# Kernel optimization log

Measured on AMD Instinct MI355X. Metric: run time of the kernel, lower is better.

The kernel has to match this reference:

```python
import jax, jax.numpy as jnp
import numpy as np

EPS = 1e-5

def layernorm2d(x, w, b):
    # nn.LayerNorm([T, C]): normalize jointly over last two dims, affine shape [T, C]
    mu = jnp.mean(x, axis=(-2, -1), keepdims=True)
    var = jnp.mean(jnp.square(x - mu), axis=(-2, -1), keepdims=True)
    return (x - mu) * jax.lax.rsqrt(var + EPS) * w + b


def setup_inputs() -> dict:
    key = jax.random.key(0)
    ks = jax.random.split(key, 10)
    B, T, C = 64, 512, 512
    s = 0.02
    inputs = jax.random.normal(ks[0], (B, T, C), dtype=jnp.float32)
    ln1_w = jnp.ones((T, C), dtype=jnp.float32)
    ln1_b = jnp.zeros((T, C), dtype=jnp.float32)
    ln2_w = jnp.ones((T, C), dtype=jnp.float32)
    ln2_b = jnp.zeros((T, C), dtype=jnp.float32)
    # TriU: row i holds the Linear(i+1,1) weights for prefix 0..i -> lower-triangular [T,T]
    tri_M = jax.random.normal(ks[1], (T, T), dtype=jnp.float32) * s
    tri_b = jax.random.normal(ks[2], (T,), dtype=jnp.float32) * s
    d1_w = jax.random.normal(ks[3], (C, C), dtype=jnp.float32) * s  # dense_1: out = x @ d1_w.T + d1_b
    d1_b = jax.random.normal(ks[4], (C,), dtype=jnp.float32) * s
    d2_w = jax.random.normal(ks[5], (C, C), dtype=jnp.float32) * s
    d2_b = jax.random.normal(ks[6], (C,), dtype=jnp.float32) * s
    return {"inputs": inputs, "ln1_w": ln1_w, "ln1_b": ln1_b,
            "ln2_w": ln2_w, "ln2_b": ln2_b,
            "tri_M": tri_M, "tri_b": tri_b,
            "d1_w": d1_w, "d1_b": d1_b, "d2_w": d2_w, "d2_b": d2_b}


def reference(inputs, ln1_w, ln1_b, ln2_w, ln2_b, tri_M, tri_b, d1_w, d1_b, d2_w, d2_b):
    # x: [B, T, C]
    x = layernorm2d(inputs, ln1_w, ln1_b)
    # TriU time mixer: out[b,i,c] = sum_{j<=i} M[i,j] * x[b,j,c] + tri_b[i]
    M = jnp.tril(tri_M)
    x = jnp.einsum('it,btc->bic', M, x) + tri_b[None, :, None]
    x = layernorm2d(x + inputs, ln2_w, ln2_b)
    # channel mixer MLP (dropout = 0)
    h = jax.nn.gelu(jnp.einsum('btc,hc->bth', x, d1_w) + d1_b, approximate=False)
    y = jnp.einsum('bth,ch->btc', h, d2_w) + d2_b
    return x + y
```

## Files before the change

### kernel.cpp

```cpp
#include <hip/hip_runtime.h>
#include <hip/hip_bf16.h>
#include <math.h>


#define B_ 64
#define T_ 512
#define C_ 512
#define TC_ (T_ * C_)
static_assert(TC_ == 262144, "");

typedef __attribute__((ext_vector_type(8))) short bf16x8;
typedef __attribute__((ext_vector_type(4))) float f32x4;

__device__ __forceinline__ unsigned short f2bf(float f) {
  union { float f; unsigned u; } v; v.f = f;
  unsigned r = v.u + 0x7FFF + ((v.u >> 16) & 1);
  return (unsigned short)(r >> 16);
}
__device__ __forceinline__ float bf2f(unsigned short h) {
  union { unsigned u; float f; } v; v.u = ((unsigned)h) << 16; return v.f;
}

__device__ __forceinline__ void load16_lds(const void* gsrc, void* ldst) {
  __builtin_amdgcn_global_load_lds(
      (const __attribute__((address_space(1))) unsigned int*)gsrc,
      (__attribute__((address_space(3))) unsigned int*)ldst,
      16, 0, 0);
}

__global__ __launch_bounds__(256) void prep(
    const float* __restrict__ triM, const float* __restrict__ d1w,
    const float* __restrict__ d2w, unsigned short* __restrict__ Mb,
    unsigned short* __restrict__ W1b, unsigned short* __restrict__ W2b,
    const float* __restrict__ x, float* __restrict__ red1p,
    float* __restrict__ red2) {
  if (blockIdx.x < 1024) {
    if (blockIdx.x == 0 && threadIdx.x < 128) red2[threadIdx.x] = 0.f;
    const int idx = blockIdx.x * 256 + threadIdx.x;
    const int i = idx >> 9, j = idx & 511;
    Mb[idx]  = (j <= i) ? f2bf(triM[idx]) : (unsigned short)0;
    W1b[idx] = f2bf(d1w[idx]);
    W2b[idx] = f2bf(d2w[idx]);
    return;
  }
  const int bb = blockIdx.x - 1024;
  const int b = bb >> 4, s = bb & 15;
  const float4* p = (const float4*)(x + (size_t)b * TC_) + (size_t)s * 4096;
  float s1 = 0.f, s2 = 0.f;
  for (int i = threadIdx.x; i < 4096; i += 256) {
    float4 v = p[i];
    s1 += v.x + v.y + v.z + v.w;
    s2 += v.x * v.x + v.y * v.y + v.z * v.z + v.w * v.w;
  }
#pragma unroll
  for (int o = 32; o; o >>= 1) { s1 += __shfl_down(s1, o, 64); s2 += __shfl_down(s2, o, 64); }
  __shared__ float sm[8];
  const int w = threadIdx.x >> 6, lane = threadIdx.x & 63;
  if (lane == 0) { sm[w * 2] = s1; sm[w * 2 + 1] = s2; }
  __syncthreads();
  if (threadIdx.x == 0) {
    float a = 0.f, c = 0.f;
    for (int i = 0; i < 4; ++i) { a += sm[2 * i]; c += sm[2 * i + 1]; }
    red1p[bb * 2] = a;
    red1p[bb * 2 + 1] = c;
  }
}

__global__ __launch_bounds__(256) void ln1_norm_t(
    const float* __restrict__ x, const float* __restrict__ w,
    const float* __restrict__ bvec, const float* __restrict__ red1p,
    unsigned short* __restrict__ XnT) {
  __shared__ unsigned short tile[64][65];
  const int b = blockIdx.z;
  const int t0 = blockIdx.y * 64;
  const int c0 = blockIdx.x * 64;
  float s1 = 0.f, s2 = 0.f;
#pragma unroll
  for (int i = 0; i < 16; ++i) {
    s1 += red1p[(b * 16 + i) * 2];
    s2 += red1p[(b * 16 + i) * 2 + 1];
  }
  const float mu = s1 * (1.f / TC_);
  const float rstd = rsqrtf(s2 * (1.f / TC_) - mu * mu + 1e-5f);
  const int tid = threadIdx.x;
  const int r = tid >> 4;
  const int cg = (tid & 15) * 4;
#pragma unroll
  for (int rr = 0; rr < 4; ++rr) {
    const int t = t0 + rr * 16 + r;
    const float4 xv = *(const float4*)&x[((size_t)b * T_ + t) * C_ + c0 + cg];
    const float4 wv = *(const float4*)&w[(size_t)t * C_ + c0 + cg];
    const float4 bv = *(const float4*)&bvec[(size_t)t * C_ + c0 + cg];
    tile[rr * 16 + r][cg + 0] = f2bf((xv.x - mu) * rstd * wv.x + bv.x);
    tile[rr * 16 + r][cg + 1] = f2bf((xv.y - mu) * rstd * wv.y + bv.y);
    tile[rr * 16 + r][cg + 2] = f2bf((xv.z - mu) * rstd * wv.z + bv.z);
    tile[rr * 16 + r][cg + 3] = f2bf((xv.w - mu) * rstd * wv.w + bv.w);
  }
  __syncthreads();
  const int cl = tid >> 2;
  const int tg = (tid & 3) * 16;
  alignas(16) unsigned short tmp[16];
#pragma unroll
  for (int j = 0; j < 16; ++j) tmp[j] = tile[tg + j][cl];
  unsigned short* o = &XnT[((size_t)b * C_ + c0 + cl) * T_ + t0 + tg];
  *(uint4*)&o[0] = *(const uint4*)&tmp[0];
  *(uint4*)&o[8] = *(const uint4*)&tmp[8];
}

__device__ __forceinline__ void stage_tile64(
    const unsigned short* __restrict__ Ag, const unsigned short* __restrict__ Bg,
    int k0, unsigned short* As, unsigned short* Bs, int tid) {
#pragma unroll
  for (int j = 0; j < 2; ++j) {
    const int c = tid + 512 * j;
    const int row = c >> 3;
    const int l = ((c & 7) ^ (row & 7)) * 8;
    load16_lds(Ag + ((size_t)row << 9) + k0 + l, As + c * 8);
    load16_lds(Bg + ((size_t)row << 9) + k0 + l, Bs + c * 8);
  }
}

__device__ __forceinline__ void mfma_tile64(
    const unsigned short* __restrict__ As, const unsigned short* __restrict__ Bs,
    int arow, int brow, int quad, int xk, f32x4 acc[4][2]) {
#pragma unroll
  for (int ks = 0; ks < 2; ++ks) {
    const int co = (((ks * 4 + quad) ^ xk) * 8);
    bf16x8 af[4], bfr[2];
#pragma unroll
    for (int m = 0; m < 4; ++m)
      af[m] = *(const bf16x8*)&As[arow + m * 1024 + co];
#pragma unroll
    for (int n = 0; n < 2; ++n)
      bfr[n] = *(const bf16x8*)&Bs[brow + n * 1024 + co];
    __builtin_amdgcn_s_setprio(1);
#pragma unroll
    for (int m = 0; m < 4; ++m)
#pragma unroll
      for (int n = 0; n < 2; ++n)
        acc[m][n] = __builtin_amdgcn_mfma_f32_16x16x32_bf16(af[m], bfr[n], acc[m][n], 0, 0, 0);
    __builtin_amdgcn_s_setprio(0);
  }
}

__device__ __forceinline__ void gemm_mainloop64(
    const unsigned short* __restrict__ Ag, const unsigned short* __restrict__ Bg,
    int ktiles,
    unsigned short* lds, f32x4 acc[4][2], int tid) {
  const int lane = tid & 63;
  const int w = tid >> 6;
  const int wm = w >> 2, wn = w & 3;
  const int m16 = lane & 15, quad = lane >> 4;
  unsigned short* A0 = lds;
  unsigned short* B0 = lds + 8192;
  unsigned short* A1 = lds + 16384;
  unsigned short* B1 = lds + 24576;
  const int arow = (wm * 64 + m16) * 64;
  const int brow = (wn * 32 + m16) * 64;
  const int xk = m16 & 7;
  stage_tile64(Ag, Bg, 0, A0, B0, tid);
  __syncthreads();
  for (int kt = 0; kt < ktiles; kt += 2) {
    stage_tile64(Ag, Bg, (kt + 1) * 64, A1, B1, tid);
    mfma_tile64(A0, B0, arow, brow, quad, xk, acc);
    __syncthreads();
    if (kt + 2 < ktiles)
      stage_tile64(Ag, Bg, (kt + 2) * 64, A0, B0, tid);
    mfma_tile64(A1, B1, arow, brow, quad, xk, acc);
    __syncthreads();
  }
}

__device__ __forceinline__ int xcd_swizzle_1024(int bid) {
  return ((bid & 7) << 7) | (bid >> 3);
}

__global__ __launch_bounds__(512, 4) void gemm_mixer(
    const unsigned short* __restrict__ Mb, const unsigned short* __restrict__ XnT,
    const float* __restrict__ trib, const float* __restrict__ inp,
    unsigned short* __restrict__ Z, float* __restrict__ red2) {
  __shared__ __align__(16) unsigned short lds[32768];
  const int swz = xcd_swizzle_1024((int)blockIdx.x);
  const int b = swz >> 4;
  const int i0 = ((swz >> 2) & 3) * 128;
  const int c0 = (swz & 3) * 128;
  f32x4 acc[4][2];
#pragma unroll
  for (int m = 0; m < 4; ++m)
#pragma unroll
    for (int n = 0; n < 2; ++n) acc[m][n] = (f32x4){0.f, 0.f, 0.f, 0.f};
  gemm_mainloop64(Mb + (size_t)i0 * T_, XnT + (size_t)b * TC_ + (size_t)c0 * T_,
                  (i0 >> 6) + 2, lds, acc, (int)threadIdx.x);
  const int tid = threadIdx.x, lane = tid & 63, w = tid >> 6;
  const int wm = w >> 2, wn = w & 3, m16 = lane & 15, quad = lane >> 4;
  const int rbase = i0 + wm * 64, cbase = c0 + wn * 32;
  float s1 = 0.f, s2 = 0.f;
#pragma unroll
  for (int m = 0; m < 4; ++m) {
#pragma unroll
    for (int g = 0; g < 4; ++g) {
      const int i = rbase + m * 16 + quad * 4 + g;
      const float tb = trib[i];
      const float* inrow = &inp[((size_t)b * T_ + i) * C_];
      unsigned short* zrow = &Z[((size_t)b * T_ + i) * C_];
#pragma unroll
      for (int n = 0; n < 2; ++n) {
        const int ch = cbase + n * 16 + m16;
        const float v = acc[m][n][g] + tb + inrow[ch];
        zrow[ch] = f2bf(v);
        s1 += v; s2 += v * v;
      }
    }
  }
#pragma unroll
  for (int o = 32; o; o >>= 1) { s1 += __shfl_down(s1, o, 64); s2 += __shfl_down(s2, o, 64); }
  __shared__ float smf[16];
  if (lane == 0) { smf[w * 2] = s1; smf[w * 2 + 1] = s2; }
  __syncthreads();
  if (tid == 0) {
    float a = 0.f, c2 = 0.f;
    for (int i = 0; i < 8; ++i) { a += smf[2 * i]; c2 += smf[2 * i + 1]; }
    atomicAdd(&red2[b * 2], a);
    atomicAdd(&red2[b * 2 + 1], c2);
  }
}

__global__ __launch_bounds__(256) void ln2_norm(
    const unsigned short* __restrict__ Z, const float* __restrict__ red2,
    const float* __restrict__ w, const float* __restrict__ bvec,
    unsigned short* __restrict__ X2) {
  const size_t e = ((size_t)blockIdx.x * 256 + threadIdx.x) * 8;
  const int b = (int)(e >> 18);
  const int tc = (int)(e & (TC_ - 1));
  const float mu = red2[b * 2] * (1.f / TC_);
  const float rstd = rsqrtf(red2[b * 2 + 1] * (1.f / TC_) - mu * mu + 1e-5f);
  uint4 zp = *(const uint4*)&Z[e];
  const unsigned short* zs = (const unsigned short*)&zp;
  alignas(16) float wv[8], bb[8];
  *(float4*)&wv[0] = *(const float4*)&w[tc];
  *(float4*)&wv[4] = *(const float4*)&w[tc + 4];
  *(float4*)&bb[0] = *(const float4*)&bvec[tc];
  *(float4*)&bb[4] = *(const float4*)&bvec[tc + 4];
  alignas(16) unsigned short o[8];
#pragma unroll
  for (int j = 0; j < 8; ++j)
    o[j] = f2bf((bf2f(zs[j]) - mu) * rstd * wv[j] + bb[j]);
  *(uint4*)&X2[e] = *(const uint4*)&o[0];
}

__global__ __launch_bounds__(512, 4) void gemm_d1(
    const unsigned short* __restrict__ X2, const unsigned short* __restrict__ W1b,
    const float* __restrict__ d1b, unsigned short* __restrict__ H) {
  __shared__ __align__(16) unsigned short lds[32768];
  const int swz = xcd_swizzle_1024((int)blockIdx.x);
  const int i0 = (swz & 255) * 128;
  const int n0 = (swz >> 8) * 128;
  f32x4 acc[4][2];
#pragma unroll
  for (int m = 0; m < 4; ++m)
#pragma unroll
    for (int n = 0; n < 2; ++n) acc[m][n] = (f32x4){0.f, 0.f, 0.f, 0.f};
  gemm_mainloop64(X2 + (size_t)i0 * C_, W1b + (size_t)n0 * C_, 8, lds, acc,
                  (int)threadIdx.x);
  const int tid = threadIdx.x, lane = tid & 63, w = tid >> 6;
  const int wm = w >> 2, wn = w & 3, m16 = lane & 15, quad = lane >> 4;
  const int rbase = i0 + wm * 64, cbase = n0 + wn * 32;
#pragma unroll
  for (int m = 0; m < 4; ++m) {
#pragma unroll
    for (int g = 0; g < 4; ++g) {
      const int row = rbase + m * 16 + quad * 4 + g;
#pragma unroll
      for (int n = 0; n < 2; ++n) {
        const int col = cbase + n * 16 + m16;
        const float v = acc[m][n][g] + d1b[col];
        const float gl = 0.5f * v * (1.0f + erff(v * 0.70710678118654752f));
        H[(size_t)row * C_ + col] = f2bf(gl);
      }
    }
  }
}

__global__ __launch_bounds__(512, 4) void gemm_d2(
    const unsigned short* __restrict__ H, const unsigned short* __restrict__ W2b,
    const float* __restrict__ d2b, const unsigned short* __restrict__ X2,
    float* __restrict__ out) {
  __shared__ __align__(16) unsigned short lds[32768];
  const int swz = xcd_swizzle_1024((int)blockIdx.x);
  const int i0 = (swz & 255) * 128;
  const int n0 = (swz >> 8) * 128;
  f32x4 acc[4][2];
#pragma unroll
  for (int m = 0; m < 4; ++m)
#pragma unroll
    for (int n = 0; n < 2; ++n) acc[m][n] = (f32x4){0.f, 0.f, 0.f, 0.f};
  gemm_mainloop64(H + (size_t)i0 * C_, W2b + (size_t)n0 * C_, 8, lds, acc,
                  (int)threadIdx.x);
  const int tid = threadIdx.x, lane = tid & 63, w = tid >> 6;
  const int wm = w >> 2, wn = w & 3, m16 = lane & 15, quad = lane >> 4;
  const int rbase = i0 + wm * 64, cbase = n0 + wn * 32;
#pragma unroll
  for (int m = 0; m < 4; ++m) {
#pragma unroll
    for (int g = 0; g < 4; ++g) {
      const int row = rbase + m * 16 + quad * 4 + g;
#pragma unroll
      for (int n = 0; n < 2; ++n) {
        const int col = cbase + n * 16 + m16;
        out[(size_t)row * C_ + col] =
            acc[m][n][g] + d2b[col] + bf2f(X2[(size_t)row * C_ + col]);
      }
    }
  }
}

extern "C" void kernel_launch(void* const* d_in, const int* in_sizes, int n_in,
                              void* d_out, int out_size, void* d_ws, size_t ws_size,
                              hipStream_t stream) {
  const float* inp  = (const float*)d_in[0];
  const float* ln1w = (const float*)d_in[1];
  const float* ln1b = (const float*)d_in[2];
  const float* ln2w = (const float*)d_in[3];
  const float* ln2b = (const float*)d_in[4];
  const float* triM = (const float*)d_in[5];
  const float* trib = (const float*)d_in[6];
  const float* d1w  = (const float*)d_in[7];
  const float* d1b  = (const float*)d_in[8];
  const float* d2w  = (const float*)d_in[9];
  const float* d2b  = (const float*)d_in[10];
  float* out = (float*)d_out;

  char* ws = (char*)d_ws;
  float* red1p = (float*)ws;
  float* red2  = (float*)(ws + 8192);
  unsigned short* Mb  = (unsigned short*)(ws + 16384);
  unsigned short* W1b = Mb + TC_;
  unsigned short* W2b = W1b + TC_;
  unsigned short* XnT = W2b + TC_;
  unsigned short* Z   = XnT + (size_t)B_ * TC_;
  unsigned short* X2  = Z + (size_t)B_ * TC_;
  unsigned short* H   = X2 + (size_t)B_ * TC_;

  prep<<<2048, 256, 0, stream>>>(triM, d1w, d2w, Mb, W1b, W2b, inp, red1p, red2);
  ln1_norm_t<<<dim3(8, 8, B_), 256, 0, stream>>>(inp, ln1w, ln1b, red1p, XnT);
  gemm_mixer<<<1024, 512, 0, stream>>>(Mb, XnT, trib, inp, Z, red2);
  ln2_norm<<<8192, 256, 0, stream>>>(Z, red2, ln2w, ln2b, X2);
  gemm_d1<<<1024, 512, 0, stream>>>(X2, W1b, d1b, H);
  gemm_d2<<<1024, 512, 0, stream>>>(H, W2b, d2b, X2, out);
}
```

Before: 248.1 us.

## Use BK=128 single LDS buffer with register-staged global prefetch in GEMMs

Replaces the double-buffered BK=64 async global-to-LDS pipeline with a single-buffered BK=128 tile. The next tile is prefetched into registers during the MFMA phase and written to LDS after a barrier, with a 16-way XOR swizzle. This halves the number of K iterations and barriers per tile. In exchange it adds VGPR pressure from the register staging and a second barrier per iteration. It also gives up the direct global_load_lds path for every tile after the first.

```diff
diff --git a/kernel.cpp b/kernel.cpp
--- a/kernel.cpp
+++ b/kernel.cpp
@@ -107,67 +107,67 @@
   *(uint4*)&o[8] = *(const uint4*)&tmp[8];
 }
 
-__device__ __forceinline__ void stage_tile64(
-    const unsigned short* __restrict__ Ag, const unsigned short* __restrict__ Bg,
-    int k0, unsigned short* As, unsigned short* Bs, int tid) {
-#pragma unroll
-  for (int j = 0; j < 2; ++j) {
-    const int c = tid + 512 * j;
-    const int row = c >> 3;
-    const int l = ((c & 7) ^ (row & 7)) * 8;
-    load16_lds(Ag + ((size_t)row << 9) + k0 + l, As + c * 8);
-    load16_lds(Bg + ((size_t)row << 9) + k0 + l, Bs + c * 8);
-  }
-}
-
-__device__ __forceinline__ void mfma_tile64(
-    const unsigned short* __restrict__ As, const unsigned short* __restrict__ Bs,
-    int arow, int brow, int quad, int xk, f32x4 acc[4][2]) {
-#pragma unroll
-  for (int ks = 0; ks < 2; ++ks) {
-    const int co = (((ks * 4 + quad) ^ xk) * 8);
-    bf16x8 af[4], bfr[2];
-#pragma unroll
-    for (int m = 0; m < 4; ++m)
-      af[m] = *(const bf16x8*)&As[arow + m * 1024 + co];
-#pragma unroll
-    for (int n = 0; n < 2; ++n)
-      bfr[n] = *(const bf16x8*)&Bs[brow + n * 1024 + co];
-    __builtin_amdgcn_s_setprio(1);
-#pragma unroll
-    for (int m = 0; m < 4; ++m)
-#pragma unroll
-      for (int n = 0; n < 2; ++n)
-        acc[m][n] = __builtin_amdgcn_mfma_f32_16x16x32_bf16(af[m], bfr[n], acc[m][n], 0, 0, 0);
-    __builtin_amdgcn_s_setprio(0);
-  }
-}
-
-__device__ __forceinline__ void gemm_mainloop64(
+__device__ __forceinline__ void gemm_mainloop_bk128(
     const unsigned short* __restrict__ Ag, const unsigned short* __restrict__ Bg,
     int ktiles,
-    unsigned short* lds, f32x4 acc[4][2], int tid) {
-  const int lane = tid & 63;
-  const int w = tid >> 6;
+    unsigned short* As, unsigned short* Bs, f32x4 acc[4][2], int tid) {
+  const int lane = tid & 63, w = tid >> 6;
   const int wm = w >> 2, wn = w & 3;
   const int m16 = lane & 15, quad = lane >> 4;
-  unsigned short* A0 = lds;
-  unsigned short* B0 = lds + 8192;
-  unsigned short* A1 = lds + 16384;
-  unsigned short* B1 = lds + 24576;
-  const int arow = (wm * 64 + m16) * 64;
-  const int brow = (wn * 32 + m16) * 64;
-  const int xk = m16 & 7;
-  stage_tile64(Ag, Bg, 0, A0, B0, tid);
+  const int arow = (wm * 64 + m16) * 128;
+  const int brow = (wn * 32 + m16) * 128;
+  int goff[4];
+#pragma unroll
+  for (int j = 0; j < 4; ++j) {
+    const int c = tid + 512 * j;
+    const int row = c >> 4;
+    goff[j] = (row << 9) + (((c & 15) ^ (row & 15)) * 8);
+  }
+#pragma unroll
+  for (int j = 0; j < 4; ++j) {
+    const int c = tid + 512 * j;
+    load16_lds(Ag + goff[j], As + c * 8);
+    load16_lds(Bg + goff[j], Bs + c * 8);
+  }
   __syncthreads();
-  for (int kt = 0; kt < ktiles; kt += 2) {
-    stage_tile64(Ag, Bg, (kt + 1) * 64, A1, B1, tid);
-    mfma_tile64(A0, B0, arow, brow, quad, xk, acc);
+  uint4 rA[4], rB[4];
+  for (int kt = 0; kt < ktiles; ++kt) {
+    const int k1 = (kt + 1) * 128;
+    if (kt + 1 < ktiles) {
+#pragma unroll
+      for (int j = 0; j < 4; ++j) {
+        rA[j] = *(const uint4*)(Ag + goff[j] + k1);
+        rB[j] = *(const uint4*)(Bg + goff[j] + k1);
+      }
+    }
+#pragma unroll
+    for (int ks = 0; ks < 4; ++ks) {
+      const int co = (((ks * 4 + quad) ^ m16) * 8);
+      bf16x8 af[4], bfr[2];
+#pragma unroll
+      for (int m = 0; m < 4; ++m)
+        af[m] = *(const bf16x8*)&As[arow + m * 2048 + co];
+#pragma unroll
+      for (int n = 0; n < 2; ++n)
+        bfr[n] = *(const bf16x8*)&Bs[brow + n * 2048 + co];
+      __builtin_amdgcn_s_setprio(1);
+#pragma unroll
+      for (int m = 0; m < 4; ++m)
+#pragma unroll
+        for (int n = 0; n < 2; ++n)
+          acc[m][n] = __builtin_amdgcn_mfma_f32_16x16x32_bf16(af[m], bfr[n], acc[m][n], 0, 0, 0);
+      __builtin_amdgcn_s_setprio(0);
+    }
     __syncthreads();
-    if (kt + 2 < ktiles)
-      stage_tile64(Ag, Bg, (kt + 2) * 64, A0, B0, tid);
-    mfma_tile64(A1, B1, arow, brow, quad, xk, acc);
-    __syncthreads();
+    if (kt + 1 < ktiles) {
+#pragma unroll
+      for (int j = 0; j < 4; ++j) {
+        const int c = tid + 512 * j;
+        *(uint4*)(As + c * 8) = rA[j];
+        *(uint4*)(Bs + c * 8) = rB[j];
+      }
+      __syncthreads();
+    }
   }
 }
 
@@ -189,8 +189,8 @@
   for (int m = 0; m < 4; ++m)
 #pragma unroll
     for (int n = 0; n < 2; ++n) acc[m][n] = (f32x4){0.f, 0.f, 0.f, 0.f};
-  gemm_mainloop64(Mb + (size_t)i0 * T_, XnT + (size_t)b * TC_ + (size_t)c0 * T_,
-                  (i0 >> 6) + 2, lds, acc, (int)threadIdx.x);
+  gemm_mainloop_bk128(Mb + (size_t)i0 * T_, XnT + (size_t)b * TC_ + (size_t)c0 * T_,
+                      (i0 >> 7) + 1, lds, lds + 16384, acc, (int)threadIdx.x);
   const int tid = threadIdx.x, lane = tid & 63, w = tid >> 6;
   const int wm = w >> 2, wn = w & 3, m16 = lane & 15, quad = lane >> 4;
   const int rbase = i0 + wm * 64, cbase = c0 + wn * 32;
@@ -260,8 +260,8 @@
   for (int m = 0; m < 4; ++m)
 #pragma unroll
     for (int n = 0; n < 2; ++n) acc[m][n] = (f32x4){0.f, 0.f, 0.f, 0.f};
-  gemm_mainloop64(X2 + (size_t)i0 * C_, W1b + (size_t)n0 * C_, 8, lds, acc,
-                  (int)threadIdx.x);
+  gemm_mainloop_bk128(X2 + (size_t)i0 * C_, W1b + (size_t)n0 * C_, 4,
+                      lds, lds + 16384, acc, (int)threadIdx.x);
   const int tid = threadIdx.x, lane = tid & 63, w = tid >> 6;
   const int wm = w >> 2, wn = w & 3, m16 = lane & 15, quad = lane >> 4;
   const int rbase = i0 + wm * 64, cbase = n0 + wn * 32;
@@ -294,8 +294,8 @@
   for (int m = 0; m < 4; ++m)
 #pragma unroll
     for (int n = 0; n < 2; ++n) acc[m][n] = (f32x4){0.f, 0.f, 0.f, 0.f};
-  gemm_mainloop64(H + (size_t)i0 * C_, W2b + (size_t)n0 * C_, 8, lds, acc,
-                  (int)threadIdx.x);
+  gemm_mainloop_bk128(H + (size_t)i0 * C_, W2b + (size_t)n0 * C_, 4,
+                      lds, lds + 16384, acc, (int)threadIdx.x);
   const int tid = threadIdx.x, lane = tid & 63, w = tid >> 6;
   const int wm = w >> 2, wn = w & 3, m16 = lane & 15, quad = lane >> 4;
   const int rbase = i0 + wm * 64, cbase = n0 + wn * 32;
```

Measured after the change: 409.1 us. +64.9%, slower.

## Use BK=128 GEMM mainloop with B fragments read directly from global into registers

Applied to the files above, without the earlier changes.

Adds a new GEMM mainloop for the two dense layers that stages only the activation tile in LDS, with a K-tile of 128 and XOR swizzling, and double-buffers it. The weight fragments are loaded straight from global memory (cache-resident) into registers, so B no longer goes through LDS. This halves the number of K iterations and barriers and cuts LDS traffic. In exchange it adds register pressure and uncoalesced global loads for B that may stall the MFMA stream. It also raises MFMA wave priority.

```diff
diff --git a/kernel.cpp b/kernel.cpp
--- a/kernel.cpp
+++ b/kernel.cpp
@@ -171,6 +171,62 @@
   }
 }
 
+__device__ __forceinline__ void gemm_bk128_breg(
+    const unsigned short* __restrict__ Ag, const unsigned short* __restrict__ Bg,
+    int ktiles,
+    unsigned short* As,
+    f32x4 acc[4][2], int tid) {
+  const int lane = tid & 63, w = tid >> 6;
+  const int wm = w >> 2, wn = w & 3;
+  const int m16 = lane & 15, quad = lane >> 4;
+  const int arow = (wm * 64 + m16) * 128;
+  const unsigned short* brow0 = Bg + (size_t)(wn * 32 + m16) * 512;
+  const unsigned short* brow1 = Bg + (size_t)(wn * 32 + 16 + m16) * 512;
+  int gofs[4];
+#pragma unroll
+  for (int j = 0; j < 4; ++j) {
+    const int c = tid + 512 * j;
+    const int row = c >> 4;
+    gofs[j] = (row << 9) + (((c & 15) ^ (row & 15)) * 8);
+  }
+#pragma unroll
+  for (int j = 0; j < 4; ++j)
+    load16_lds(Ag + gofs[j], As + (tid + 512 * j) * 8);
+  __syncthreads();
+  for (int kt = 0; kt < ktiles; ++kt) {
+    unsigned short* Ac = As + (kt & 1) * 16384;
+    unsigned short* An = As + ((kt + 1) & 1) * 16384;
+    bf16x8 bf[4][2];
+    const int kb = kt * 128;
+#pragma unroll
+    for (int ks = 0; ks < 4; ++ks) {
+      bf[ks][0] = *(const bf16x8*)&brow0[kb + ks * 32 + quad * 8];
+      bf[ks][1] = *(const bf16x8*)&brow1[kb + ks * 32 + quad * 8];
+    }
+    if (kt + 1 < ktiles) {
+#pragma unroll
+      for (int j = 0; j < 4; ++j)
+        load16_lds(Ag + (kt + 1) * 128 + gofs[j], An + (tid + 512 * j) * 8);
+    }
+#pragma unroll
+    for (int ks = 0; ks < 4; ++ks) {
+      const int co = (((ks * 4 + quad) ^ m16) * 8);
+      bf16x8 af[4];
+#pragma unroll
+      for (int m = 0; m < 4; ++m)
+        af[m] = *(const bf16x8*)&Ac[arow + m * 2048 + co];
+      __builtin_amdgcn_s_setprio(1);
+#pragma unroll
+      for (int m = 0; m < 4; ++m)
+#pragma unroll
+        for (int n = 0; n < 2; ++n)
+          acc[m][n] = __builtin_amdgcn_mfma_f32_16x16x32_bf16(af[m], bf[ks][n], acc[m][n], 0, 0, 0);
+      __builtin_amdgcn_s_setprio(0);
+    }
+    __syncthreads();
+  }
+}
+
 __device__ __forceinline__ int xcd_swizzle_1024(int bid) {
   return ((bid & 7) << 7) | (bid >> 3);
 }
@@ -260,7 +316,7 @@
   for (int m = 0; m < 4; ++m)
 #pragma unroll
     for (int n = 0; n < 2; ++n) acc[m][n] = (f32x4){0.f, 0.f, 0.f, 0.f};
-  gemm_mainloop64(X2 + (size_t)i0 * C_, W1b + (size_t)n0 * C_, 8, lds, acc,
+  gemm_bk128_breg(X2 + (size_t)i0 * C_, W1b + (size_t)n0 * C_, 4, lds, acc,
                   (int)threadIdx.x);
   const int tid = threadIdx.x, lane = tid & 63, w = tid >> 6;
   const int wm = w >> 2, wn = w & 3, m16 = lane & 15, quad = lane >> 4;
@@ -294,7 +350,7 @@
   for (int m = 0; m < 4; ++m)
 #pragma unroll
     for (int n = 0; n < 2; ++n) acc[m][n] = (f32x4){0.f, 0.f, 0.f, 0.f};
-  gemm_mainloop64(H + (size_t)i0 * C_, W2b + (size_t)n0 * C_, 8, lds, acc,
+  gemm_bk128_breg(H + (size_t)i0 * C_, W2b + (size_t)n0 * C_, 4, lds, acc,
                   (int)threadIdx.x);
   const int tid = threadIdx.x, lane = tid & 63, w = tid >> 6;
   const int wm = w >> 2, wn = w & 3, m16 = lane & 15, quad = lane >> 4;
```

After: 277.5 us. 1.12x slower.

## Rework GEMM mainloop sync, reuse workspace buffers, and remap MLP tiles per XCD

Applied to the files above, without the earlier changes.

The GEMM mainloop now runs one k-tile per iteration. It issues the next tile's async LDS loads, then uses explicit vmcnt/lgkmcnt waits and raw s_barrier with sched_barrier fences, so that global loads overlap the MFMA work with tighter synchronisation. LN2 now normalizes in place into Z, and H reuses the XnT buffer, which shrinks the workspace footprint and may improve cache reuse. MLP GEMM blocks are remapped so each XCD owns a contiguous range of row tiles, aiming for better L2 locality of the A rows. The hand-written waitcnt values (vmcnt(4)) depend on how many loads stage_tile64 issues, so a mismatch could cause races.

```diff
diff --git a/kernel.cpp b/kernel.cpp
--- a/kernel.cpp
+++ b/kernel.cpp
@@ -159,15 +159,26 @@
   const int brow = (wn * 32 + m16) * 64;
   const int xk = m16 & 7;
   stage_tile64(Ag, Bg, 0, A0, B0, tid);
-  __syncthreads();
-  for (int kt = 0; kt < ktiles; kt += 2) {
-    stage_tile64(Ag, Bg, (kt + 1) * 64, A1, B1, tid);
-    mfma_tile64(A0, B0, arow, brow, quad, xk, acc);
-    __syncthreads();
-    if (kt + 2 < ktiles)
-      stage_tile64(Ag, Bg, (kt + 2) * 64, A0, B0, tid);
-    mfma_tile64(A1, B1, arow, brow, quad, xk, acc);
-    __syncthreads();
+  for (int kt = 0; kt < ktiles; ++kt) {
+    unsigned short* Ac = (kt & 1) ? A1 : A0;
+    unsigned short* Bc = (kt & 1) ? B1 : B0;
+    unsigned short* An = (kt & 1) ? A0 : A1;
+    unsigned short* Bn = (kt & 1) ? B0 : B1;
+    if (kt + 1 < ktiles) {
+      stage_tile64(Ag, Bg, (kt + 1) * 64, An, Bn, tid);
+      __builtin_amdgcn_sched_barrier(0);
+      asm volatile("s_waitcnt vmcnt(4)" ::: "memory");
+    } else {
+      __builtin_amdgcn_sched_barrier(0);
+      asm volatile("s_waitcnt vmcnt(0)" ::: "memory");
+    }
+    __builtin_amdgcn_s_barrier();
+    __builtin_amdgcn_sched_barrier(0);
+    mfma_tile64(Ac, Bc, arow, brow, quad, xk, acc);
+    __builtin_amdgcn_sched_barrier(0);
+    asm volatile("s_waitcnt lgkmcnt(0)" ::: "memory");
+    __builtin_amdgcn_s_barrier();
+    __builtin_amdgcn_sched_barrier(0);
   }
 }
 
@@ -226,9 +237,8 @@
 }
 
 __global__ __launch_bounds__(256) void ln2_norm(
-    const unsigned short* __restrict__ Z, const float* __restrict__ red2,
-    const float* __restrict__ w, const float* __restrict__ bvec,
-    unsigned short* __restrict__ X2) {
+    unsigned short* Z, const float* __restrict__ red2,
+    const float* __restrict__ w, const float* __restrict__ bvec) {
   const size_t e = ((size_t)blockIdx.x * 256 + threadIdx.x) * 8;
   const int b = (int)(e >> 18);
   const int tc = (int)(e & (TC_ - 1));
@@ -245,16 +255,22 @@
 #pragma unroll
   for (int j = 0; j < 8; ++j)
     o[j] = f2bf((bf2f(zs[j]) - mu) * rstd * wv[j] + bb[j]);
-  *(uint4*)&X2[e] = *(const uint4*)&o[0];
+  *(uint4*)&Z[e] = *(const uint4*)&o[0];
+}
+
+__device__ __forceinline__ void mlp_tile_map(int bid, int* i0, int* n0) {
+  const int xcd = bid & 7;
+  const int idx = bid >> 3;
+  *i0 = (xcd * 32 + (idx & 31)) * 128;
+  *n0 = (idx >> 5) * 128;
 }
 
 __global__ __launch_bounds__(512, 4) void gemm_d1(
     const unsigned short* __restrict__ X2, const unsigned short* __restrict__ W1b,
     const float* __restrict__ d1b, unsigned short* __restrict__ H) {
   __shared__ __align__(16) unsigned short lds[32768];
-  const int swz = xcd_swizzle_1024((int)blockIdx.x);
-  const int i0 = (swz & 255) * 128;
-  const int n0 = (swz >> 8) * 128;
+  int i0, n0;
+  mlp_tile_map((int)blockIdx.x, &i0, &n0);
   f32x4 acc[4][2];
 #pragma unroll
   for (int m = 0; m < 4; ++m)
@@ -286,9 +302,8 @@
     const float* __restrict__ d2b, const unsigned short* __restrict__ X2,
     float* __restrict__ out) {
   __shared__ __align__(16) unsigned short lds[32768];
-  const int swz = xcd_swizzle_1024((int)blockIdx.x);
-  const int i0 = (swz & 255) * 128;
-  const int n0 = (swz >> 8) * 128;
+  int i0, n0;
+  mlp_tile_map((int)blockIdx.x, &i0, &n0);
   f32x4 acc[4][2];
 #pragma unroll
   for (int m = 0; m < 4; ++m)
@@ -338,13 +353,13 @@
   unsigned short* W2b = W1b + TC_;
   unsigned short* XnT = W2b + TC_;
   unsigned short* Z   = XnT + (size_t)B_ * TC_;
-  unsigned short* X2  = Z + (size_t)B_ * TC_;
-  unsigned short* H   = X2 + (size_t)B_ * TC_;
+  unsigned short* H   = XnT;
+  unsigned short* X2  = Z;
 
   prep<<<2048, 256, 0, stream>>>(triM, d1w, d2w, Mb, W1b, W2b, inp, red1p, red2);
   ln1_norm_t<<<dim3(8, 8, B_), 256, 0, stream>>>(inp, ln1w, ln1b, red1p, XnT);
   gemm_mixer<<<1024, 512, 0, stream>>>(Mb, XnT, trib, inp, Z, red2);
-  ln2_norm<<<8192, 256, 0, stream>>>(Z, red2, ln2w, ln2b, X2);
+  ln2_norm<<<8192, 256, 0, stream>>>(Z, red2, ln2w, ln2b);
   gemm_d1<<<1024, 512, 0, stream>>>(X2, W1b, d1b, H);
   gemm_d2<<<1024, 512, 0, stream>>>(H, W2b, d2b, X2, out);
 }
```

Result: slower. 258.2 us (+4.1%).
